# Performance work log

Measured on AMD Instinct MI355X. Metric: run time of the kernel, lower is better.

Reference implementation:

```python
import jax, jax.numpy as jnp
import numpy as np

N = 50000      # nodes
E = 800000     # edges (before self loops)
D_IN = 256     # input feature dim
H = 64         # hidden dim
HEADS = 4
NEG_SLOPE = 0.2  # PyG GATConv default


def setup_inputs() -> dict:
    key = jax.random.key(0)
    ks = jax.random.split(key, 24)

    def w(k, shape, fan_in):
        return jax.random.normal(k, shape, jnp.float32) / np.sqrt(fan_in)

    inp = {
        "x": jax.random.normal(ks[0], (N, D_IN), jnp.float32),
        "edge_index": jax.random.randint(ks[1], (2, E), 0, N, jnp.int64),
        # GCN layers
        "W0": w(ks[2], (D_IN, H), D_IN), "b0": jnp.zeros((H,), jnp.float32),
        "W1": w(ks[3], (H, H), H),       "b1": jnp.zeros((H,), jnp.float32),
        "W2": w(ks[4], (H, H), H),       "b2": jnp.zeros((H,), jnp.float32),
        # GAT
        "Wg": w(ks[5], (H, HEADS * H), H),
        "att_src": w(ks[6], (HEADS, H), H),
        "att_dst": w(ks[7], (HEADS, H), H),
        "bg": jnp.zeros((H,), jnp.float32),
        # classifier MLP: H -> H//2 -> 2
        "Wc1": w(ks[8], (H, H // 2), H),   "bc1": jnp.zeros((H // 2,), jnp.float32),
        "Wc2": w(ks[9], (H // 2, 2), H // 2), "bc2": jnp.zeros((2,), jnp.float32),
        # reconstructor MLP: H -> H -> D_IN
        "Wr1": w(ks[10], (H, H), H),       "br1": jnp.zeros((H,), jnp.float32),
        "Wr2": w(ks[11], (H, D_IN), H),    "br2": jnp.zeros((D_IN,), jnp.float32),
    }
    return inp


def reference(x, edge_index, W0, b0, W1, b1, W2, b2,
              Wg, att_src, att_dst, bg,
              Wc1, bc1, Wc2, bc2, Wr1, br1, Wr2, br2):
    # add self loops (PyG default for both GCNConv and GATConv)
    loops = jnp.arange(N, dtype=edge_index.dtype)
    src = jnp.concatenate([edge_index[0], loops])  # [E+N]
    dst = jnp.concatenate([edge_index[1], loops])

    # symmetric GCN normalization: deg^-1/2[src] * deg^-1/2[dst]
    deg = jax.ops.segment_sum(jnp.ones_like(src, jnp.float32), dst, num_segments=N)
    dinv = jnp.where(deg > 0, jax.lax.rsqrt(deg), 0.0)
    norm = dinv[src] * dinv[dst]  # [E+N]

    def gcn(h, W, b):
        msg = (h @ W)[src] * norm[:, None]          # gather + scale
        return jax.ops.segment_sum(msg, dst, num_segments=N) + b

    # stacked GCN with residuals (dropout inactive in eval)
    h = jax.nn.relu(gcn(x, W0, b0))                 # [N, H]
    h = h + jax.nn.relu(gcn(h, W1, b1))
    h = h + jax.nn.relu(gcn(h, W2, b2))

    # GAT layer, 4 heads, concat=False -> mean over heads
    xg = (h @ Wg).reshape(N, HEADS, H)              # [N, heads, H]
    a_s = jnp.einsum('nhf,hf->nh', xg, att_src)     # [N, heads]
    a_d = jnp.einsum('nhf,hf->nh', xg, att_dst)
    e = jax.nn.leaky_relu(a_s[src] + a_d[dst], NEG_SLOPE)  # [E+N, heads]
    m = jax.ops.segment_max(e, dst, num_segments=N)        # segment softmax
    ex = jnp.exp(e - m[dst])
    s = jax.ops.segment_sum(ex, dst, num_segments=N)
    alpha = ex / s[dst]                                     # [E+N, heads]
    hg = jax.ops.segment_sum(xg[src] * alpha[:, :, None], dst, num_segments=N)
    hg = hg.mean(axis=1) + bg                                # [N, H]

    # global mean pool (batch is None)
    h_global = hg.mean(axis=0, keepdims=True)                # [1, H]
    cls = jax.nn.relu(h_global @ Wc1 + bc1) @ Wc2 + bc2      # [1, 2]
    rec = jax.nn.relu(hg @ Wr1 + br1) @ Wr2 + br2            # [N, D_IN]
    return cls, rec, hg
```

## Files before the change

kernel.cpp:

```cpp
#include <hip/hip_runtime.h>

#define DIN 256
#define HD 64
#define NHEAD 4

static inline int cdiv(long a, long b) { return (int)((a + b - 1) / b); }

typedef __attribute__((ext_vector_type(8))) short bf16x8;
typedef __attribute__((ext_vector_type(4))) float f32x4;

__global__ __launch_bounds__(256) void k_count(const int* __restrict__ dst,
                                               int* __restrict__ cnt, int E) {
  int i = blockIdx.x * 256 + threadIdx.x;
  if (i < E) atomicAdd(&cnt[dst[i]], 1);
}

__global__ __launch_bounds__(256) void k_bsum(const int* __restrict__ cnt,
                                              int* __restrict__ bsum, int n) {
  __shared__ int sd[256];
  int i = blockIdx.x * 256 + threadIdx.x;
  sd[threadIdx.x] = (i < n) ? cnt[i] + 1 : 0;
  __syncthreads();
  for (int o = 128; o > 0; o >>= 1) {
    if (threadIdx.x < o) sd[threadIdx.x] += sd[threadIdx.x + o];
    __syncthreads();
  }
  if (threadIdx.x == 0) bsum[blockIdx.x] = sd[0];
}

__global__ __launch_bounds__(256) void k_rowptr(const int* __restrict__ cnt,
                                                const int* __restrict__ bsum,
                                                int* __restrict__ row_ptr,
                                                int* __restrict__ cursor,
                                                float* __restrict__ dinv,
                                                float* __restrict__ gsum,
                                                int n, int total, int B) {
  __shared__ int sb[256];
  __shared__ int sd[256];
  int t = threadIdx.x;
  sb[t] = (t < B) ? bsum[t] : 0;
  __syncthreads();
  for (int o = 1; o < 256; o <<= 1) {
    int x = (t >= o) ? sb[t - o] : 0;
    __syncthreads();
    sb[t] += x;
    __syncthreads();
  }
  int boff = (blockIdx.x > 0) ? sb[blockIdx.x - 1] : 0;
  int i = blockIdx.x * 256 + t;
  int v = (i < n) ? cnt[i] + 1 : 0;
  sd[t] = v;
  __syncthreads();
  for (int o = 1; o < 256; o <<= 1) {
    int x = (t >= o) ? sd[t - o] : 0;
    __syncthreads();
    sd[t] += x;
    __syncthreads();
  }
  if (i < n) {
    int rp = boff + sd[t] - v;
    row_ptr[i] = rp;
    cursor[i] = rp;
    dinv[i] = rsqrtf((float)v);
  }
  if (i == n - 1) row_ptr[n] = total;
  if (blockIdx.x == 0 && t < 64) gsum[t] = 0.f;
}

__global__ __launch_bounds__(256) void k_csrfill(const int* __restrict__ src,
                                                 const int* __restrict__ dst,
                                                 int* __restrict__ cursor,
                                                 int* __restrict__ csr_src, int E, int n) {
  int e = blockIdx.x * 256 + threadIdx.x;
  if (e < E) {
    int pos = atomicAdd(&cursor[dst[e]], 1);
    csr_src[pos] = src[e];
  } else if (e < E + n) {
    int i = e - E;
    int pos = atomicAdd(&cursor[i], 1);
    csr_src[pos] = i;
  }
}

__device__ __forceinline__ unsigned short f2bf(float f) {
  unsigned u = __float_as_uint(f);
  u += 0x7FFFu + ((u >> 16) & 1u);
  return (unsigned short)(u >> 16);
}
__device__ __forceinline__ float bflo(unsigned u) { return __uint_as_float(u << 16); }
__device__ __forceinline__ float bfhi(unsigned u) { return __uint_as_float(u & 0xFFFF0000u); }

template <int KIN, int KOUT, int ATT>
__global__ __launch_bounds__(256, 4) void k_gmfma(const float* __restrict__ A,
                                                  const float* __restrict__ W,
                                                  unsigned short* __restrict__ c16, int n,
                                                  const float* __restrict__ attS,
                                                  const float* __restrict__ attD,
                                                  float* __restrict__ a_s,
                                                  float* __restrict__ a_d) {
  __shared__ unsigned short As[64][64];
  __shared__ unsigned short Wt[64][64];
  const int tid = threadIdx.x;
  const int m0 = blockIdx.x * 64;
  const int n0 = blockIdx.y * 64;
  const int lane = tid & 63;
  const int wid = tid >> 6;
  const int wm = wid * 16;
  const int fr = lane & 15;
  const int fg = lane >> 4;
  f32x4 acc[4] = {{0.f, 0.f, 0.f, 0.f},
                  {0.f, 0.f, 0.f, 0.f},
                  {0.f, 0.f, 0.f, 0.f},
                  {0.f, 0.f, 0.f, 0.f}};

  for (int k0 = 0; k0 < KIN; k0 += 64) {
    {
      int row = tid >> 3;
      int g = tid & 7;
#pragma unroll
      for (int q = 0; q < 2; ++q, row += 32) {
        int gr = m0 + row;
        gr = gr < n ? gr : n - 1;
        const float* ap = A + (size_t)gr * KIN + k0 + g * 8;
        float4 f0 = *(const float4*)ap;
        float4 f1 = *(const float4*)(ap + 4);
        uint4 pk;
        pk.x = (unsigned)f2bf(f0.x) | ((unsigned)f2bf(f0.y) << 16);
        pk.y = (unsigned)f2bf(f0.z) | ((unsigned)f2bf(f0.w) << 16);
        pk.z = (unsigned)f2bf(f1.x) | ((unsigned)f2bf(f1.y) << 16);
        pk.w = (unsigned)f2bf(f1.z) | ((unsigned)f2bf(f1.w) << 16);
        *(uint4*)&As[row][(g ^ (row & 7)) * 8] = pk;
      }
    }
    {
      int col = tid & 63;
      int kb = (tid >> 6) * 16;
      unsigned pk[8];
#pragma unroll
      for (int i = 0; i < 8; ++i) {
        float lo = W[(size_t)(k0 + kb + 2 * i) * KOUT + n0 + col];
        float hi = W[(size_t)(k0 + kb + 2 * i + 1) * KOUT + n0 + col];
        pk[i] = (unsigned)f2bf(lo) | ((unsigned)f2bf(hi) << 16);
      }
      int g0 = kb >> 3;
      uint4 w0; w0.x = pk[0]; w0.y = pk[1]; w0.z = pk[2]; w0.w = pk[3];
      uint4 w1; w1.x = pk[4]; w1.y = pk[5]; w1.z = pk[6]; w1.w = pk[7];
      *(uint4*)&Wt[col][((g0) ^ (col & 7)) * 8] = w0;
      *(uint4*)&Wt[col][((g0 + 1) ^ (col & 7)) * 8] = w1;
    }
    __syncthreads();
#pragma unroll
    for (int ks = 0; ks < 2; ++ks) {
      int ga = ks * 4 + fg;
      bf16x8 af = *(const bf16x8*)&As[wm + fr][(ga ^ (fr & 7)) * 8];
#pragma unroll
      for (int nt = 0; nt < 4; ++nt) {
        bf16x8 bfr = *(const bf16x8*)&Wt[nt * 16 + fr][(ga ^ (fr & 7)) * 8];
        acc[nt] = __builtin_amdgcn_mfma_f32_16x16x32_bf16(af, bfr, acc[nt], 0, 0, 0);
      }
    }
    __syncthreads();
  }

#pragma unroll
  for (int nt = 0; nt < 4; ++nt) {
#pragma unroll
    for (int r = 0; r < 4; ++r) {
      int row = m0 + wm + fg * 4 + r;
      if (row < n) c16[(size_t)row * KOUT + n0 + nt * 16 + fr] = f2bf(acc[nt][r]);
    }
  }
  if (ATT) {
    float attsv[4], attdv[4];
#pragma unroll
    for (int nt = 0; nt < 4; ++nt) {
      attsv[nt] = attS[n0 + nt * 16 + fr];
      attdv[nt] = attD[n0 + nt * 16 + fr];
    }
#pragma unroll
    for (int r = 0; r < 4; ++r) {
      float ps = acc[0][r] * attsv[0] + acc[1][r] * attsv[1] +
                 acc[2][r] * attsv[2] + acc[3][r] * attsv[3];
      float pd = acc[0][r] * attdv[0] + acc[1][r] * attdv[1] +
                 acc[2][r] * attdv[2] + acc[3][r] * attdv[3];
#pragma unroll
      for (int o = 1; o < 16; o <<= 1) {
        ps += __shfl_xor(ps, o);
        pd += __shfl_xor(pd, o);
      }
      int row = m0 + wm + fg * 4 + r;
      if (fr == 0 && row < n) {
        a_s[row * NHEAD + blockIdx.y] = ps;
        a_d[row * NHEAD + blockIdx.y] = pd;
      }
    }
  }
}

__global__ __launch_bounds__(256, 4) void k_rec(const float* __restrict__ hg,
                                                const float* __restrict__ Wr1,
                                                const float* __restrict__ br1,
                                                const float* __restrict__ Wr2,
                                                const float* __restrict__ br2,
                                                float* __restrict__ gsum,
                                                float* __restrict__ rec,
                                                int n) {
  __shared__ unsigned short As[64][64];
  __shared__ unsigned short Ws[64][64];
  __shared__ unsigned short Ts[64][64];
  __shared__ float gs[64];
  const int tid = threadIdx.x;
  const int m0 = blockIdx.x * 64;
  const int lane = tid & 63;
  const int wid = tid >> 6;
  const int wm = wid * 16;
  const int fr = lane & 15, fg = lane >> 4;

  if (tid < 64) gs[tid] = 0.f;
  __syncthreads();

  {
    int row = tid >> 3, g = tid & 7;
#pragma unroll
    for (int q = 0; q < 2; ++q, row += 32) {
      int gr = m0 + row;
      bool valid = gr < n;
      int cr = valid ? gr : n - 1;
      const float* hp = hg + (size_t)cr * HD + g * 8;
      float2 f0 = *(const float2*)hp;
      float2 f1 = *(const float2*)(hp + 2);
      float2 f2 = *(const float2*)(hp + 4);
      float2 f3 = *(const float2*)(hp + 6);
      uint4 pk;
      pk.x = (unsigned)f2bf(f0.x) | ((unsigned)f2bf(f0.y) << 16);
      pk.y = (unsigned)f2bf(f1.x) | ((unsigned)f2bf(f1.y) << 16);
      pk.z = (unsigned)f2bf(f2.x) | ((unsigned)f2bf(f2.y) << 16);
      pk.w = (unsigned)f2bf(f3.x) | ((unsigned)f2bf(f3.y) << 16);
      *(uint4*)&As[row][(g ^ (row & 7)) * 8] = pk;
      if (valid) {
        atomicAdd(&gs[g * 8 + 0], f0.x); atomicAdd(&gs[g * 8 + 1], f0.y);
        atomicAdd(&gs[g * 8 + 2], f1.x); atomicAdd(&gs[g * 8 + 3], f1.y);
        atomicAdd(&gs[g * 8 + 4], f2.x); atomicAdd(&gs[g * 8 + 5], f2.y);
        atomicAdd(&gs[g * 8 + 6], f3.x); atomicAdd(&gs[g * 8 + 7], f3.y);
      }
    }
  }
  {
    int col = tid & 63;
    int kb = (tid >> 6) * 16;
    unsigned pk[8];
#pragma unroll
    for (int i = 0; i < 8; ++i) {
      float lo = Wr1[(size_t)(kb + 2 * i) * HD + col];
      float hi = Wr1[(size_t)(kb + 2 * i + 1) * HD + col];
      pk[i] = (unsigned)f2bf(lo) | ((unsigned)f2bf(hi) << 16);
    }
    int g0 = kb >> 3;
    uint4 w0; w0.x = pk[0]; w0.y = pk[1]; w0.z = pk[2]; w0.w = pk[3];
    uint4 w1; w1.x = pk[4]; w1.y = pk[5]; w1.z = pk[6]; w1.w = pk[7];
    *(uint4*)&Ws[col][((g0) ^ (col & 7)) * 8] = w0;
    *(uint4*)&Ws[col][((g0 + 1) ^ (col & 7)) * 8] = w1;
  }
  __syncthreads();
  if (tid < 64) atomicAdd(&gsum[tid], gs[tid]);

  {
    f32x4 acc[4] = {{0.f, 0.f, 0.f, 0.f}, {0.f, 0.f, 0.f, 0.f},
                    {0.f, 0.f, 0.f, 0.f}, {0.f, 0.f, 0.f, 0.f}};
#pragma unroll
    for (int ks = 0; ks < 2; ++ks) {
      int ga = ks * 4 + fg;
      bf16x8 af = *(const bf16x8*)&As[wm + fr][(ga ^ (fr & 7)) * 8];
#pragma unroll
      for (int nt = 0; nt < 4; ++nt) {
        bf16x8 bfr = *(const bf16x8*)&Ws[nt * 16 + fr][(ga ^ (fr & 7)) * 8];
        acc[nt] = __builtin_amdgcn_mfma_f32_16x16x32_bf16(af, bfr, acc[nt], 0, 0, 0);
      }
    }
#pragma unroll
    for (int nt = 0; nt < 4; ++nt) {
#pragma unroll
      for (int r = 0; r < 4; ++r) {
        int row = wm + fg * 4 + r;
        int col = nt * 16 + fr;
        float v = acc[nt][r] + br1[col];
        v = v > 0.f ? v : 0.f;
        Ts[row][(((col >> 3) ^ (row & 7)) * 8) + (col & 7)] = f2bf(v);
      }
    }
  }

  for (int cg = 0; cg < 4; ++cg) {
    __syncthreads();
    {
      int col = tid & 63;
      int kb = (tid >> 6) * 16;
      unsigned pk[8];
#pragma unroll
      for (int i = 0; i < 8; ++i) {
        float lo = Wr2[(size_t)(kb + 2 * i) * 256 + cg * 64 + col];
        float hi = Wr2[(size_t)(kb + 2 * i + 1) * 256 + cg * 64 + col];
        pk[i] = (unsigned)f2bf(lo) | ((unsigned)f2bf(hi) << 16);
      }
      int g0 = kb >> 3;
      uint4 w0; w0.x = pk[0]; w0.y = pk[1]; w0.z = pk[2]; w0.w = pk[3];
      uint4 w1; w1.x = pk[4]; w1.y = pk[5]; w1.z = pk[6]; w1.w = pk[7];
      *(uint4*)&Ws[col][((g0) ^ (col & 7)) * 8] = w0;
      *(uint4*)&Ws[col][((g0 + 1) ^ (col & 7)) * 8] = w1;
    }
    __syncthreads();
    f32x4 acc[4] = {{0.f, 0.f, 0.f, 0.f}, {0.f, 0.f, 0.f, 0.f},
                    {0.f, 0.f, 0.f, 0.f}, {0.f, 0.f, 0.f, 0.f}};
#pragma unroll
    for (int ks = 0; ks < 2; ++ks) {
      int ga = ks * 4 + fg;
      bf16x8 af = *(const bf16x8*)&Ts[wm + fr][(ga ^ (fr & 7)) * 8];
#pragma unroll
      for (int nt = 0; nt < 4; ++nt) {
        bf16x8 bfr = *(const bf16x8*)&Ws[nt * 16 + fr][(ga ^ (fr & 7)) * 8];
        acc[nt] = __builtin_amdgcn_mfma_f32_16x16x32_bf16(af, bfr, acc[nt], 0, 0, 0);
      }
    }
#pragma unroll
    for (int nt = 0; nt < 4; ++nt) {
#pragma unroll
      for (int r = 0; r < 4; ++r) {
        int row = m0 + wm + fg * 4 + r;
        int col = cg * 64 + nt * 16 + fr;
        if (row < n) rec[(size_t)row * 256 + col] = acc[nt][r] + br2[col];
      }
    }
  }
}

__global__ __launch_bounds__(256) void k_agg16(const unsigned short* __restrict__ P16,
                                               const int* __restrict__ csr_src,
                                               const int* __restrict__ row_ptr,
                                               const float* __restrict__ dinv,
                                               const float* __restrict__ bias,
                                               const float* __restrict__ resid,
                                               float* __restrict__ out, int n) {
  int node = (blockIdx.x * 256 + threadIdx.x) >> 6;
  int lane = threadIdx.x & 63;
  if (node >= n) return;
  int beg = row_ptr[node], end = row_ptr[node + 1];
  int es = lane >> 3;
  int fo = (lane & 7) * 8;
  float a[8] = {};
  for (int i = beg + es; i < end; i += 8) {
    int s = csr_src[i];
    float d = dinv[s];
    uint4 v = *(const uint4*)(P16 + (size_t)s * HD + fo);
    a[0] = fmaf(bflo(v.x), d, a[0]); a[1] = fmaf(bfhi(v.x), d, a[1]);
    a[2] = fmaf(bflo(v.y), d, a[2]); a[3] = fmaf(bfhi(v.y), d, a[3]);
    a[4] = fmaf(bflo(v.z), d, a[4]); a[5] = fmaf(bfhi(v.z), d, a[5]);
    a[6] = fmaf(bflo(v.w), d, a[6]); a[7] = fmaf(bfhi(v.w), d, a[7]);
  }
#pragma unroll
  for (int o = 8; o < 64; o <<= 1) {
#pragma unroll
    for (int k = 0; k < 8; ++k) a[k] += __shfl_xor(a[k], o);
  }
  if (lane < 8) {
    float dn = dinv[node];
    float4 b0 = *(const float4*)(bias + fo);
    float4 b1 = *(const float4*)(bias + fo + 4);
    float o0[8];
    o0[0] = a[0] * dn + b0.x; o0[1] = a[1] * dn + b0.y;
    o0[2] = a[2] * dn + b0.z; o0[3] = a[3] * dn + b0.w;
    o0[4] = a[4] * dn + b1.x; o0[5] = a[5] * dn + b1.y;
    o0[6] = a[6] * dn + b1.z; o0[7] = a[7] * dn + b1.w;
#pragma unroll
    for (int k = 0; k < 8; ++k) o0[k] = o0[k] > 0.f ? o0[k] : 0.f;
    if (resid) {
      float4 r0 = *(const float4*)(resid + (size_t)node * HD + fo);
      float4 r1 = *(const float4*)(resid + (size_t)node * HD + fo + 4);
      o0[0] += r0.x; o0[1] += r0.y; o0[2] += r0.z; o0[3] += r0.w;
      o0[4] += r1.x; o0[5] += r1.y; o0[6] += r1.z; o0[7] += r1.w;
    }
    float4 w0; w0.x = o0[0]; w0.y = o0[1]; w0.z = o0[2]; w0.w = o0[3];
    float4 w1; w1.x = o0[4]; w1.y = o0[5]; w1.z = o0[6]; w1.w = o0[7];
    *(float4*)(out + (size_t)node * HD + fo) = w0;
    *(float4*)(out + (size_t)node * HD + fo + 4) = w1;
  }
}

__device__ __forceinline__ float leaky(float v) { return v > 0.f ? v : 0.2f * v; }

__global__ __launch_bounds__(256) void k_gat(const unsigned short* __restrict__ xg16,
                                             const float* __restrict__ a_s,
                                             const float* __restrict__ a_d,
                                             const int* __restrict__ csr_src,
                                             const int* __restrict__ row_ptr,
                                             float* __restrict__ galpha,
                                             const float* __restrict__ bg,
                                             float* __restrict__ hg,
                                             int n) {
  __shared__ float4 ew[4][128];
  const int wid = threadIdx.x >> 6;
  const int node = (blockIdx.x * 256 + threadIdx.x) >> 6;
  const int lane = threadIdx.x & 63;
  if (node >= n) return;
  const int beg = row_ptr[node], end = row_ptr[node + 1];
  const bool uselds = (end - beg) <= 128;
  float4 ad = ((const float4*)a_d)[node];

  float m0 = -1e30f, m1 = -1e30f, m2 = -1e30f, m3 = -1e30f;
  float4 e0, e1;
  const int i0 = beg + lane, i1 = beg + lane + 64;
  if (uselds) {
    if (i0 < end) {
      int s = csr_src[i0];
      float4 as = ((const float4*)a_s)[s];
      e0.x = leaky(as.x + ad.x); e0.y = leaky(as.y + ad.y);
      e0.z = leaky(as.z + ad.z); e0.w = leaky(as.w + ad.w);
      m0 = e0.x; m1 = e0.y; m2 = e0.z; m3 = e0.w;
    }
    if (i1 < end) {
      int s = csr_src[i1];
      float4 as = ((const float4*)a_s)[s];
      e1.x = leaky(as.x + ad.x); e1.y = leaky(as.y + ad.y);
      e1.z = leaky(as.z + ad.z); e1.w = leaky(as.w + ad.w);
      m0 = fmaxf(m0, e1.x); m1 = fmaxf(m1, e1.y);
      m2 = fmaxf(m2, e1.z); m3 = fmaxf(m3, e1.w);
    }
  } else {
    for (int i = i0; i < end; i += 64) {
      int s = csr_src[i];
      float4 as = ((const float4*)a_s)[s];
      float4 e;
      e.x = leaky(as.x + ad.x); e.y = leaky(as.y + ad.y);
      e.z = leaky(as.z + ad.z); e.w = leaky(as.w + ad.w);
      ((float4*)galpha)[i] = e;
      m0 = fmaxf(m0, e.x); m1 = fmaxf(m1, e.y);
      m2 = fmaxf(m2, e.z); m3 = fmaxf(m3, e.w);
    }
    __threadfence();
  }
#pragma unroll
  for (int o = 32; o > 0; o >>= 1) {
    m0 = fmaxf(m0, __shfl_xor(m0, o));
    m1 = fmaxf(m1, __shfl_xor(m1, o));
    m2 = fmaxf(m2, __shfl_xor(m2, o));
    m3 = fmaxf(m3, __shfl_xor(m3, o));
  }

  float s0 = 0.f, s1 = 0.f, s2 = 0.f, s3 = 0.f;
  if (uselds) {
    if (i0 < end) {
      float4 ex;
      ex.x = expf(e0.x - m0); ex.y = expf(e0.y - m1);
      ex.z = expf(e0.z - m2); ex.w = expf(e0.w - m3);
      ew[wid][i0 - beg] = ex;
      s0 += ex.x; s1 += ex.y; s2 += ex.z; s3 += ex.w;
    }
    if (i1 < end) {
      float4 ex;
      ex.x = expf(e1.x - m0); ex.y = expf(e1.y - m1);
      ex.z = expf(e1.z - m2); ex.w = expf(e1.w - m3);
      ew[wid][i1 - beg] = ex;
      s0 += ex.x; s1 += ex.y; s2 += ex.z; s3 += ex.w;
    }
  } else {
    for (int i = i0; i < end; i += 64) {
      float4 e = ((const float4*)galpha)[i];
      float4 ex;
      ex.x = expf(e.x - m0); ex.y = expf(e.y - m1);
      ex.z = expf(e.z - m2); ex.w = expf(e.w - m3);
      ((float4*)galpha)[i] = ex;
      s0 += ex.x; s1 += ex.y; s2 += ex.z; s3 += ex.w;
    }
    __threadfence();
  }
#pragma unroll
  for (int o = 32; o > 0; o >>= 1) {
    s0 += __shfl_xor(s0, o);
    s1 += __shfl_xor(s1, o);
    s2 += __shfl_xor(s2, o);
    s3 += __shfl_xor(s3, o);
  }
  float r0 = 0.25f / s0, r1 = 0.25f / s1, r2 = 0.25f / s2, r3 = 0.25f / s3;

  const int hl = lane & 31;
  const int hw = lane >> 5;
  const int head = hl >> 3;
  float a[8] = {}, b[8] = {};

#define GATHER8(ACC, S, AL)                                                     \
  {                                                                             \
    uint4 v = *(const uint4*)(xg16 + (size_t)(S) * 256 + hl * 8);               \
    ACC[0] = fmaf(bflo(v.x), AL, ACC[0]); ACC[1] = fmaf(bfhi(v.x), AL, ACC[1]); \
    ACC[2] = fmaf(bflo(v.y), AL, ACC[2]); ACC[3] = fmaf(bfhi(v.y), AL, ACC[3]); \
    ACC[4] = fmaf(bflo(v.z), AL, ACC[4]); ACC[5] = fmaf(bfhi(v.z), AL, ACC[5]); \
    ACC[6] = fmaf(bflo(v.w), AL, ACC[6]); ACC[7] = fmaf(bfhi(v.w), AL, ACC[7]); \
  }

#define P3_BODY(ALPHA_AT)                                  \
  {                                                        \
    int i = beg + hw;                                      \
    for (; i + 2 < end; i += 4) {                          \
      int sA = csr_src[i], sB = csr_src[i + 2];            \
      float alA = ALPHA_AT(i), alB = ALPHA_AT(i + 2);      \
      GATHER8(a, sA, alA)                                  \
      GATHER8(b, sB, alB)                                  \
    }                                                      \
    for (; i < end; i += 2) {                              \
      int s = csr_src[i];                                  \
      float al = ALPHA_AT(i);                              \
      GATHER8(a, s, al)                                    \
    }                                                      \
  }

  if (uselds) {
    const float* ap = (const float*)&ew[wid][0];
#define AL_LDS(idx) ap[((idx) - beg) * 4 + head]
    P3_BODY(AL_LDS)
#undef AL_LDS
  } else {
#define AL_GBL(idx) galpha[(size_t)(idx) * 4 + head]
    P3_BODY(AL_GBL)
#undef AL_GBL
  }
#undef P3_BODY
#undef GATHER8

  float rh = head == 0 ? r0 : head == 1 ? r1 : head == 2 ? r2 : r3;
  float t[8];
#pragma unroll
  for (int k = 0; k < 8; ++k) {
    t[k] = a[k] + b[k];
    t[k] += __shfl_xor(t[k], 32);
    t[k] *= rh;
    t[k] += __shfl_xor(t[k], 8);
    t[k] += __shfl_xor(t[k], 16);
  }
  if (lane < 8) {
    int f0 = lane * 8;
    float o0[8];
#pragma unroll
    for (int k = 0; k < 8; ++k) o0[k] = t[k] + bg[f0 + k];
    float2 p0; p0.x = o0[0]; p0.y = o0[1];
    float2 p1; p1.x = o0[2]; p1.y = o0[3];
    float2 p2; p2.x = o0[4]; p2.y = o0[5];
    float2 p3; p3.x = o0[6]; p3.y = o0[7];
    *(float2*)(hg + (size_t)node * HD + f0) = p0;
    *(float2*)(hg + (size_t)node * HD + f0 + 2) = p1;
    *(float2*)(hg + (size_t)node * HD + f0 + 4) = p2;
    *(float2*)(hg + (size_t)node * HD + f0 + 6) = p3;
  }
}

__global__ __launch_bounds__(64) void k_cls(const float* __restrict__ gsum,
                                            const float* __restrict__ Wc1,
                                            const float* __restrict__ bc1,
                                            const float* __restrict__ Wc2,
                                            const float* __restrict__ bc2,
                                            float* __restrict__ out, int n) {
  __shared__ float hgl[64];
  __shared__ float t1[32];
  int t = threadIdx.x;
  hgl[t] = gsum[t] / (float)n;
  __syncthreads();
  if (t < 32) {
    float a = bc1[t];
#pragma unroll 16
    for (int f = 0; f < 64; ++f) a = fmaf(hgl[f], Wc1[f * 32 + t], a);
    t1[t] = a > 0.f ? a : 0.f;
  }
  __syncthreads();
  if (t < 2) {
    float a = bc2[t];
#pragma unroll
    for (int j = 0; j < 32; ++j) a = fmaf(t1[j], Wc2[j * 2 + t], a);
    out[t] = a;
  }
}

extern "C" void kernel_launch(void* const* d_in, const int* in_sizes, int n_in,
                              void* d_out, int out_size, void* d_ws, size_t ws_size,
                              hipStream_t stream) {
  const float* x = (const float*)d_in[0];
  const int* ei = (const int*)d_in[1];
  const float* W0 = (const float*)d_in[2];
  const float* b0 = (const float*)d_in[3];
  const float* W1 = (const float*)d_in[4];
  const float* b1 = (const float*)d_in[5];
  const float* W2 = (const float*)d_in[6];
  const float* b2 = (const float*)d_in[7];
  const float* Wg = (const float*)d_in[8];
  const float* att_src = (const float*)d_in[9];
  const float* att_dst = (const float*)d_in[10];
  const float* bg = (const float*)d_in[11];
  const float* Wc1 = (const float*)d_in[12];
  const float* bc1 = (const float*)d_in[13];
  const float* Wc2 = (const float*)d_in[14];
  const float* bc2 = (const float*)d_in[15];
  const float* Wr1 = (const float*)d_in[16];
  const float* br1 = (const float*)d_in[17];
  const float* Wr2 = (const float*)d_in[18];
  const float* br2 = (const float*)d_in[19];

  const int n = in_sizes[0] / DIN;
  const int E = in_sizes[1] / 2;
  const int nE = E + n;
  const int* src = ei;
  const int* dst = ei + E;

  float* ws = (float*)d_ws;
  size_t off = 0;
  auto alloc = [&](size_t nelems) {
    float* p = ws + off;
    off += (nelems + 63) & ~(size_t)63;
    return p;
  };
  int* CNT = (int*)alloc(n);
  int* BSUM = (int*)alloc(256);
  int* ROWP = (int*)alloc(n + 1);
  int* CURS = (int*)alloc(n);
  int* CSRS = (int*)alloc(nE);
  float* DINV = alloc(n);
  unsigned short* XG16 = (unsigned short*)alloc((size_t)n * 128);
  unsigned short* P16 = (unsigned short*)alloc((size_t)n * 32);
  float* Hb = alloc((size_t)n * HD);
  float* ASD = alloc((size_t)n * NHEAD);
  float* ADD = alloc((size_t)n * NHEAD);
  float* GALPHA = alloc((size_t)nE * NHEAD);
  float* GSUM = alloc(64);
  (void)ws_size;

  float* out = (float*)d_out;
  float* out_cls = out;
  float* out_rec = out + 2;
  float* out_hg = out + 2 + (size_t)n * 256;

  const int TB = 256;
  const int B = cdiv(n, TB);
  const int GM = cdiv(n, 64);

  hipMemsetAsync(CNT, 0, (size_t)n * sizeof(int), stream);
  k_count<<<cdiv(E, TB), TB, 0, stream>>>(dst, CNT, E);
  k_bsum<<<B, TB, 0, stream>>>(CNT, BSUM, n);
  k_rowptr<<<B, TB, 0, stream>>>(CNT, BSUM, ROWP, CURS, DINV, GSUM, n, nE, B);
  k_csrfill<<<cdiv(nE, TB), TB, 0, stream>>>(src, dst, CURS, CSRS, E, n);

  k_gmfma<256, 64, 0><<<dim3(GM, 1), TB, 0, stream>>>(x, W0, P16, n,
                                                      nullptr, nullptr, nullptr, nullptr);
  k_agg16<<<cdiv((long)n * 64, TB), TB, 0, stream>>>(P16, CSRS, ROWP, DINV, b0, nullptr, Hb, n);

  k_gmfma<64, 64, 0><<<dim3(GM, 1), TB, 0, stream>>>(Hb, W1, P16, n,
                                                     nullptr, nullptr, nullptr, nullptr);
  k_agg16<<<cdiv((long)n * 64, TB), TB, 0, stream>>>(P16, CSRS, ROWP, DINV, b1, Hb, Hb, n);

  k_gmfma<64, 64, 0><<<dim3(GM, 1), TB, 0, stream>>>(Hb, W2, P16, n,
                                                     nullptr, nullptr, nullptr, nullptr);
  k_agg16<<<cdiv((long)n * 64, TB), TB, 0, stream>>>(P16, CSRS, ROWP, DINV, b2, Hb, Hb, n);

  k_gmfma<64, 256, 1><<<dim3(GM, 4), TB, 0, stream>>>(Hb, Wg, XG16, n,
                                                      att_src, att_dst, ASD, ADD);
  k_gat<<<cdiv((long)n * 64, TB), TB, 0, stream>>>(XG16, ASD, ADD, CSRS, ROWP, GALPHA, bg,
                                                   out_hg, n);

  k_rec<<<GM, TB, 0, stream>>>(out_hg, Wr1, br1, Wr2, br2, GSUM, out_rec, n);
  k_cls<<<1, 64, 0, stream>>>(GSUM, Wc1, bc1, Wc2, bc2, out_cls, n);
}
```

Measured before the change: 342.7 us.

## Fuse GCN aggregation with the following layer's projection GEMM

Merges each GCN aggregation kernel with the next layer's bf16 MFMA projection, so aggregated rows are written to shared memory instead of round-tripping through global memory before a separate GEMM launch. Ping-pong bf16 buffers hold the projected features, and the last layer writes no fp32 hidden state, only the GAT projection and attention logits. It removes three kernel launches and one fp32 hidden read per layer. In exchange, each block has four waves walking 16 nodes sequentially, which cuts parallelism for the latency-bound gather.

```diff
diff --git a/kernel.cpp b/kernel.cpp
--- a/kernel.cpp
+++ b/kernel.cpp
@@ -90,19 +90,13 @@
 __device__ __forceinline__ float bflo(unsigned u) { return __uint_as_float(u << 16); }
 __device__ __forceinline__ float bfhi(unsigned u) { return __uint_as_float(u & 0xFFFF0000u); }
 
-template <int KIN, int KOUT, int ATT>
-__global__ __launch_bounds__(256, 4) void k_gmfma(const float* __restrict__ A,
-                                                  const float* __restrict__ W,
-                                                  unsigned short* __restrict__ c16, int n,
-                                                  const float* __restrict__ attS,
-                                                  const float* __restrict__ attD,
-                                                  float* __restrict__ a_s,
-                                                  float* __restrict__ a_d) {
+__global__ __launch_bounds__(256, 4) void k_gmfma0(const float* __restrict__ A,
+                                                   const float* __restrict__ W,
+                                                   unsigned short* __restrict__ c16, int n) {
   __shared__ unsigned short As[64][64];
   __shared__ unsigned short Wt[64][64];
   const int tid = threadIdx.x;
   const int m0 = blockIdx.x * 64;
-  const int n0 = blockIdx.y * 64;
   const int lane = tid & 63;
   const int wid = tid >> 6;
   const int wm = wid * 16;
@@ -113,7 +107,7 @@
                   {0.f, 0.f, 0.f, 0.f},
                   {0.f, 0.f, 0.f, 0.f}};
 
-  for (int k0 = 0; k0 < KIN; k0 += 64) {
+  for (int k0 = 0; k0 < 256; k0 += 64) {
     {
       int row = tid >> 3;
       int g = tid & 7;
@@ -121,7 +115,7 @@
       for (int q = 0; q < 2; ++q, row += 32) {
         int gr = m0 + row;
         gr = gr < n ? gr : n - 1;
-        const float* ap = A + (size_t)gr * KIN + k0 + g * 8;
+        const float* ap = A + (size_t)gr * 256 + k0 + g * 8;
         float4 f0 = *(const float4*)ap;
         float4 f1 = *(const float4*)(ap + 4);
         uint4 pk;
@@ -138,8 +132,8 @@
       unsigned pk[8];
 #pragma unroll
       for (int i = 0; i < 8; ++i) {
-        float lo = W[(size_t)(k0 + kb + 2 * i) * KOUT + n0 + col];
-        float hi = W[(size_t)(k0 + kb + 2 * i + 1) * KOUT + n0 + col];
+        float lo = W[(size_t)(k0 + kb + 2 * i) * HD + col];
+        float hi = W[(size_t)(k0 + kb + 2 * i + 1) * HD + col];
         pk[i] = (unsigned)f2bf(lo) | ((unsigned)f2bf(hi) << 16);
       }
       int g0 = kb >> 3;
@@ -167,33 +161,157 @@
 #pragma unroll
     for (int r = 0; r < 4; ++r) {
       int row = m0 + wm + fg * 4 + r;
-      if (row < n) c16[(size_t)row * KOUT + n0 + nt * 16 + fr] = f2bf(acc[nt][r]);
-    }
-  }
-  if (ATT) {
-    float attsv[4], attdv[4];
+      if (row < n) c16[(size_t)row * HD + nt * 16 + fr] = f2bf(acc[nt][r]);
+    }
+  }
+}
+
+template <int RESID, int WRITE_H, int WG>
+__global__ __launch_bounds__(256, 4) void k_layer(const unsigned short* __restrict__ Pin,
+                                                  const int* __restrict__ csr_src,
+                                                  const int* __restrict__ row_ptr,
+                                                  const float* __restrict__ dinv,
+                                                  const float* __restrict__ bias,
+                                                  const float* __restrict__ hin,
+                                                  float* __restrict__ hout,
+                                                  const float* __restrict__ W,
+                                                  unsigned short* __restrict__ c16,
+                                                  const float* __restrict__ attS,
+                                                  const float* __restrict__ attD,
+                                                  float* __restrict__ a_s,
+                                                  float* __restrict__ a_d, int n) {
+  __shared__ unsigned short As[64][64];
+  __shared__ unsigned short Ws[64][64];
+  const int tid = threadIdx.x, lane = tid & 63, wid = tid >> 6;
+  const int m0 = blockIdx.x * 64;
+  const int es = lane >> 3, fo = (lane & 7) * 8;
+
+  for (int j = 0; j < 16; ++j) {
+    int row = wid * 16 + j;
+    int node = m0 + row;
+    float a[8] = {};
+    if (node < n) {
+      int beg = row_ptr[node], end = row_ptr[node + 1];
+      for (int i = beg + es; i < end; i += 8) {
+        int s = csr_src[i];
+        float d = dinv[s];
+        uint4 v = *(const uint4*)(Pin + (size_t)s * HD + fo);
+        a[0] = fmaf(bflo(v.x), d, a[0]); a[1] = fmaf(bfhi(v.x), d, a[1]);
+        a[2] = fmaf(bflo(v.y), d, a[2]); a[3] = fmaf(bfhi(v.y), d, a[3]);
+        a[4] = fmaf(bflo(v.z), d, a[4]); a[5] = fmaf(bfhi(v.z), d, a[5]);
+        a[6] = fmaf(bflo(v.w), d, a[6]); a[7] = fmaf(bfhi(v.w), d, a[7]);
+      }
+    }
+#pragma unroll
+    for (int o = 8; o < 64; o <<= 1) {
+#pragma unroll
+      for (int k = 0; k < 8; ++k) a[k] += __shfl_xor(a[k], o);
+    }
+    if (lane < 8) {
+      if (node < n) {
+        float dn = dinv[node];
+        float4 b0v = *(const float4*)(bias + fo);
+        float4 b1v = *(const float4*)(bias + fo + 4);
+        float o0[8];
+        o0[0] = a[0] * dn + b0v.x; o0[1] = a[1] * dn + b0v.y;
+        o0[2] = a[2] * dn + b0v.z; o0[3] = a[3] * dn + b0v.w;
+        o0[4] = a[4] * dn + b1v.x; o0[5] = a[5] * dn + b1v.y;
+        o0[6] = a[6] * dn + b1v.z; o0[7] = a[7] * dn + b1v.w;
+#pragma unroll
+        for (int k = 0; k < 8; ++k) o0[k] = o0[k] > 0.f ? o0[k] : 0.f;
+        if (RESID) {
+          float4 r0 = *(const float4*)(hin + (size_t)node * HD + fo);
+          float4 r1 = *(const float4*)(hin + (size_t)node * HD + fo + 4);
+          o0[0] += r0.x; o0[1] += r0.y; o0[2] += r0.z; o0[3] += r0.w;
+          o0[4] += r1.x; o0[5] += r1.y; o0[6] += r1.z; o0[7] += r1.w;
+        }
+        if (WRITE_H) {
+          float4 w0; w0.x = o0[0]; w0.y = o0[1]; w0.z = o0[2]; w0.w = o0[3];
+          float4 w1; w1.x = o0[4]; w1.y = o0[5]; w1.z = o0[6]; w1.w = o0[7];
+          *(float4*)(hout + (size_t)node * HD + fo) = w0;
+          *(float4*)(hout + (size_t)node * HD + fo + 4) = w1;
+        }
+        uint4 pk;
+        pk.x = (unsigned)f2bf(o0[0]) | ((unsigned)f2bf(o0[1]) << 16);
+        pk.y = (unsigned)f2bf(o0[2]) | ((unsigned)f2bf(o0[3]) << 16);
+        pk.z = (unsigned)f2bf(o0[4]) | ((unsigned)f2bf(o0[5]) << 16);
+        pk.w = (unsigned)f2bf(o0[6]) | ((unsigned)f2bf(o0[7]) << 16);
+        *(uint4*)&As[row][((lane & 7) ^ (row & 7)) * 8] = pk;
+      } else {
+        uint4 z = {0, 0, 0, 0};
+        *(uint4*)&As[row][((lane & 7) ^ (row & 7)) * 8] = z;
+      }
+    }
+  }
+  __syncthreads();
+
+  const int wm = wid * 16, fr = lane & 15, fg = lane >> 4;
+  constexpr int KOUT = WG ? 256 : 64;
+  constexpr int NCG = WG ? 4 : 1;
+  for (int cg = 0; cg < NCG; ++cg) {
+    {
+      int col = tid & 63;
+      int kb = (tid >> 6) * 16;
+      unsigned pk[8];
+#pragma unroll
+      for (int i = 0; i < 8; ++i) {
+        float lo = W[(size_t)(kb + 2 * i) * KOUT + cg * 64 + col];
+        float hi = W[(size_t)(kb + 2 * i + 1) * KOUT + cg * 64 + col];
+        pk[i] = (unsigned)f2bf(lo) | ((unsigned)f2bf(hi) << 16);
+      }
+      int g0 = kb >> 3;
+      uint4 w0; w0.x = pk[0]; w0.y = pk[1]; w0.z = pk[2]; w0.w = pk[3];
+      uint4 w1; w1.x = pk[4]; w1.y = pk[5]; w1.z = pk[6]; w1.w = pk[7];
+      *(uint4*)&Ws[col][((g0) ^ (col & 7)) * 8] = w0;
+      *(uint4*)&Ws[col][((g0 + 1) ^ (col & 7)) * 8] = w1;
+    }
+    __syncthreads();
+    f32x4 acc[4] = {{0.f, 0.f, 0.f, 0.f}, {0.f, 0.f, 0.f, 0.f},
+                    {0.f, 0.f, 0.f, 0.f}, {0.f, 0.f, 0.f, 0.f}};
+#pragma unroll
+    for (int ks = 0; ks < 2; ++ks) {
+      int ga = ks * 4 + fg;
+      bf16x8 af = *(const bf16x8*)&As[wm + fr][(ga ^ (fr & 7)) * 8];
+#pragma unroll
+      for (int nt = 0; nt < 4; ++nt) {
+        bf16x8 bfr = *(const bf16x8*)&Ws[nt * 16 + fr][(ga ^ (fr & 7)) * 8];
+        acc[nt] = __builtin_amdgcn_mfma_f32_16x16x32_bf16(af, bfr, acc[nt], 0, 0, 0);
+      }
+    }
 #pragma unroll
     for (int nt = 0; nt < 4; ++nt) {
-      attsv[nt] = attS[n0 + nt * 16 + fr];
-      attdv[nt] = attD[n0 + nt * 16 + fr];
-    }
-#pragma unroll
-    for (int r = 0; r < 4; ++r) {
-      float ps = acc[0][r] * attsv[0] + acc[1][r] * attsv[1] +
-                 acc[2][r] * attsv[2] + acc[3][r] * attsv[3];
-      float pd = acc[0][r] * attdv[0] + acc[1][r] * attdv[1] +
-                 acc[2][r] * attdv[2] + acc[3][r] * attdv[3];
-#pragma unroll
-      for (int o = 1; o < 16; o <<= 1) {
-        ps += __shfl_xor(ps, o);
-        pd += __shfl_xor(pd, o);
-      }
-      int row = m0 + wm + fg * 4 + r;
-      if (fr == 0 && row < n) {
-        a_s[row * NHEAD + blockIdx.y] = ps;
-        a_d[row * NHEAD + blockIdx.y] = pd;
-      }
-    }
+#pragma unroll
+      for (int r = 0; r < 4; ++r) {
+        int row = m0 + wm + fg * 4 + r;
+        if (row < n) c16[(size_t)row * KOUT + cg * 64 + nt * 16 + fr] = f2bf(acc[nt][r]);
+      }
+    }
+    if (WG) {
+      float attsv[4], attdv[4];
+#pragma unroll
+      for (int nt = 0; nt < 4; ++nt) {
+        attsv[nt] = attS[cg * 64 + nt * 16 + fr];
+        attdv[nt] = attD[cg * 64 + nt * 16 + fr];
+      }
+#pragma unroll
+      for (int r = 0; r < 4; ++r) {
+        float ps = acc[0][r] * attsv[0] + acc[1][r] * attsv[1] +
+                   acc[2][r] * attsv[2] + acc[3][r] * attsv[3];
+        float pd = acc[0][r] * attdv[0] + acc[1][r] * attdv[1] +
+                   acc[2][r] * attdv[2] + acc[3][r] * attdv[3];
+#pragma unroll
+        for (int o = 1; o < 16; o <<= 1) {
+          ps += __shfl_xor(ps, o);
+          pd += __shfl_xor(pd, o);
+        }
+        int row = m0 + wm + fg * 4 + r;
+        if (fr == 0 && row < n) {
+          a_s[row * NHEAD + cg] = ps;
+          a_d[row * NHEAD + cg] = pd;
+        }
+      }
+    }
+    if (cg + 1 < NCG) __syncthreads();
   }
 }
 
@@ -330,58 +448,6 @@
         if (row < n) rec[(size_t)row * 256 + col] = acc[nt][r] + br2[col];
       }
     }
-  }
-}
-
-__global__ __launch_bounds__(256) void k_agg16(const unsigned short* __restrict__ P16,
-                                               const int* __restrict__ csr_src,
-                                               const int* __restrict__ row_ptr,
-                                               const float* __restrict__ dinv,
-                                               const float* __restrict__ bias,
-                                               const float* __restrict__ resid,
-                                               float* __restrict__ out, int n) {
-  int node = (blockIdx.x * 256 + threadIdx.x) >> 6;
-  int lane = threadIdx.x & 63;
-  if (node >= n) return;
-  int beg = row_ptr[node], end = row_ptr[node + 1];
-  int es = lane >> 3;
-  int fo = (lane & 7) * 8;
-  float a[8] = {};
-  for (int i = beg + es; i < end; i += 8) {
-    int s = csr_src[i];
-    float d = dinv[s];
-    uint4 v = *(const uint4*)(P16 + (size_t)s * HD + fo);
-    a[0] = fmaf(bflo(v.x), d, a[0]); a[1] = fmaf(bfhi(v.x), d, a[1]);
-    a[2] = fmaf(bflo(v.y), d, a[2]); a[3] = fmaf(bfhi(v.y), d, a[3]);
-    a[4] = fmaf(bflo(v.z), d, a[4]); a[5] = fmaf(bfhi(v.z), d, a[5]);
-    a[6] = fmaf(bflo(v.w), d, a[6]); a[7] = fmaf(bfhi(v.w), d, a[7]);
-  }
-#pragma unroll
-  for (int o = 8; o < 64; o <<= 1) {
-#pragma unroll
-    for (int k = 0; k < 8; ++k) a[k] += __shfl_xor(a[k], o);
-  }
-  if (lane < 8) {
-    float dn = dinv[node];
-    float4 b0 = *(const float4*)(bias + fo);
-    float4 b1 = *(const float4*)(bias + fo + 4);
-    float o0[8];
-    o0[0] = a[0] * dn + b0.x; o0[1] = a[1] * dn + b0.y;
-    o0[2] = a[2] * dn + b0.z; o0[3] = a[3] * dn + b0.w;
-    o0[4] = a[4] * dn + b1.x; o0[5] = a[5] * dn + b1.y;
-    o0[6] = a[6] * dn + b1.z; o0[7] = a[7] * dn + b1.w;
-#pragma unroll
-    for (int k = 0; k < 8; ++k) o0[k] = o0[k] > 0.f ? o0[k] : 0.f;
-    if (resid) {
-      float4 r0 = *(const float4*)(resid + (size_t)node * HD + fo);
-      float4 r1 = *(const float4*)(resid + (size_t)node * HD + fo + 4);
-      o0[0] += r0.x; o0[1] += r0.y; o0[2] += r0.z; o0[3] += r0.w;
-      o0[4] += r1.x; o0[5] += r1.y; o0[6] += r1.z; o0[7] += r1.w;
-    }
-    float4 w0; w0.x = o0[0]; w0.y = o0[1]; w0.z = o0[2]; w0.w = o0[3];
-    float4 w1; w1.x = o0[4]; w1.y = o0[5]; w1.z = o0[6]; w1.w = o0[7];
-    *(float4*)(out + (size_t)node * HD + fo) = w0;
-    *(float4*)(out + (size_t)node * HD + fo + 4) = w1;
   }
 }
 
@@ -620,7 +686,8 @@
   int* CSRS = (int*)alloc(nE);
   float* DINV = alloc(n);
   unsigned short* XG16 = (unsigned short*)alloc((size_t)n * 128);
-  unsigned short* P16 = (unsigned short*)alloc((size_t)n * 32);
+  unsigned short* P16A = (unsigned short*)alloc((size_t)n * 32);
+  unsigned short* P16B = (unsigned short*)alloc((size_t)n * 32);
   float* Hb = alloc((size_t)n * HD);
   float* ASD = alloc((size_t)n * NHEAD);
   float* ADD = alloc((size_t)n * NHEAD);
@@ -643,20 +710,14 @@
   k_rowptr<<<B, TB, 0, stream>>>(CNT, BSUM, ROWP, CURS, DINV, GSUM, n, nE, B);
   k_csrfill<<<cdiv(nE, TB), TB, 0, stream>>>(src, dst, CURS, CSRS, E, n);
 
-  k_gmfma<256, 64, 0><<<dim3(GM, 1), TB, 0, stream>>>(x, W0, P16, n,
-                                                      nullptr, nullptr, nullptr, nullptr);
-  k_agg16<<<cdiv((long)n * 64, TB), TB, 0, stream>>>(P16, CSRS, ROWP, DINV, b0, nullptr, Hb, n);
-
-  k_gmfma<64, 64, 0><<<dim3(GM, 1), TB, 0, stream>>>(Hb, W1, P16, n,
-                                                     nullptr, nullptr, nullptr, nullptr);
-  k_agg16<<<cdiv((long)n * 64, TB), TB, 0, stream>>>(P16, CSRS, ROWP, DINV, b1, Hb, Hb, n);
-
-  k_gmfma<64, 64, 0><<<dim3(GM, 1), TB, 0, stream>>>(Hb, W2, P16, n,
-                                                     nullptr, nullptr, nullptr, nullptr);
-  k_agg16<<<cdiv((long)n * 64, TB), TB, 0, stream>>>(P16, CSRS, ROWP, DINV, b2, Hb, Hb, n);
-
-  k_gmfma<64, 256, 1><<<dim3(GM, 4), TB, 0, stream>>>(Hb, Wg, XG16, n,
-                                                      att_src, att_dst, ASD, ADD);
+  k_gmfma0<<<GM, TB, 0, stream>>>(x, W0, P16A, n);
+  k_layer<0, 1, 0><<<GM, TB, 0, stream>>>(P16A, CSRS, ROWP, DINV, b0, nullptr, Hb,
+                                          W1, P16B, nullptr, nullptr, nullptr, nullptr, n);
+  k_layer<1, 1, 0><<<GM, TB, 0, stream>>>(P16B, CSRS, ROWP, DINV, b1, Hb, Hb,
+                                          W2, P16A, nullptr, nullptr, nullptr, nullptr, n);
+  k_layer<1, 0, 1><<<GM, TB, 0, stream>>>(P16A, CSRS, ROWP, DINV, b2, Hb, nullptr,
+                                          Wg, XG16, att_src, att_dst, ASD, ADD, n);
+
   k_gat<<<cdiv((long)n * 64, TB), TB, 0, stream>>>(XG16, ASD, ADD, CSRS, ROWP, GALPHA, bg,
                                                    out_hg, n);
 
```

Result: slower. 393.1 us (+14.7%).
